# Kernel tuning notes

Measured on AMD Instinct MI355X. Metric: run time of the kernel, lower is better.

Reference implementation:

```python
import jax, jax.numpy as jnp
import numpy as np

WINDOW = 8            # window_size
P = WINDOW * WINDOW   # tokens per window = 64
DIM = 256             # feature_dim (per-token channels)
HEADS = 8
HEAD_DIM = DIM // HEADS
EPS = 1e-5


def _relative_position_index():
    # Swin-style relative position index for a WINDOW x WINDOW window.
    coords = np.stack(np.meshgrid(np.arange(WINDOW), np.arange(WINDOW), indexing='ij'))  # 2,w,w
    coords = coords.reshape(2, -1)                        # 2, P
    rel = coords[:, :, None] - coords[:, None, :]          # 2, P, P
    rel = rel.transpose(1, 2, 0)                           # P, P, 2
    rel = rel + (WINDOW - 1)
    idx = rel[:, :, 0] * (2 * WINDOW - 1) + rel[:, :, 1]   # P, P
    return idx.astype(np.int32)


def setup_inputs() -> dict:
    key = jax.random.key(0)
    ks = jax.random.split(key, 8)
    B, N, D = 8, 256, P * DIM
    x = jax.random.normal(ks[0], (B, N, D), dtype=jnp.float32)
    global_noise_info = jax.random.uniform(ks[1], (B, 1, D), dtype=jnp.float32)
    norm_gamma = jnp.ones((DIM,), jnp.float32)
    norm_beta = jnp.zeros((DIM,), jnp.float32)
    s = 1.0 / np.sqrt(DIM)
    qkv_w = jax.random.normal(ks[2], (3 * DIM, DIM), dtype=jnp.float32) * s
    proj_w = jax.random.normal(ks[3], (DIM, DIM), dtype=jnp.float32) * s
    proj_b = jnp.zeros((DIM,), jnp.float32)
    n_rel = (2 * WINDOW - 1) ** 2
    rel_bias_table = jax.random.normal(ks[4], (n_rel, HEADS), dtype=jnp.float32) * 0.02
    rel_index = jnp.asarray(_relative_position_index())  # (P, P) int32
    return {
        'x': x, 'global_noise_info': global_noise_info,
        'norm_gamma': norm_gamma, 'norm_beta': norm_beta,
        'qkv_w': qkv_w, 'proj_w': proj_w, 'proj_b': proj_b,
        'rel_bias_table': rel_bias_table, 'rel_index': rel_index,
    }


def reference(x, global_noise_info, norm_gamma, norm_beta, qkv_w, proj_w, proj_b,
              rel_bias_table, rel_index):
    B, N, D = x.shape
    d = D // P
    # elementwise noise scale + window reshape: (B, N, P*d) -> (B*N, P, d)
    xw = (x * global_noise_info).reshape(B * N, P, d)
    # LayerNorm over channel dim
    mu = jnp.mean(xw, axis=-1, keepdims=True)
    var = jnp.var(xw, axis=-1, keepdims=True)
    xn = (xw - mu) * jax.lax.rsqrt(var + EPS) * norm_gamma + norm_beta
    # qkv projection (no bias)
    qkv = jnp.einsum('wpd,ed->wpe', xn, qkv_w)                    # (BN, P, 3D)
    qkv = qkv.reshape(B * N, P, 3, HEADS, HEAD_DIM)
    q, k, v = qkv[:, :, 0], qkv[:, :, 1], qkv[:, :, 2]            # (BN, P, H, hd)
    scale = HEAD_DIM ** -0.5
    scores = jnp.einsum('wphc,wqhc->whpq', q * scale, k)          # (BN, H, P, P)
    bias = rel_bias_table[rel_index]                               # (P, P, H)
    scores = scores + jnp.transpose(bias, (2, 0, 1))[None]
    attn = jax.nn.softmax(scores, axis=-1)
    out = jnp.einsum('whpq,wqhc->wphc', attn, v).reshape(B * N, P, d)
    out = jnp.einsum('wpd,ed->wpe', out, proj_w) + proj_b
    return out.reshape(B, N, D)
```

## Files before the change

### kernel.cpp

```cpp
#include <hip/hip_runtime.h>
#include <hip/hip_fp16.h>

typedef _Float16 f16;
typedef __attribute__((ext_vector_type(8)))  f16   f16x8;
typedef __attribute__((ext_vector_type(16))) float f32x16;
typedef __attribute__((ext_vector_type(4)))  float f32x4;
typedef __attribute__((ext_vector_type(2)))  unsigned int u32x2;
typedef unsigned int uint;
typedef unsigned short ushort;

#define MFMA16 __builtin_amdgcn_mfma_f32_32x32x16_f16

#define SCALE_Q 0.17677669529663687f

#define XN_ROW   264
#define XN_BYTES (64 * XN_ROW * 2)
#define Q_OFF    XN_BYTES
#define QK_ROW   40
#define QK_HEAD  (64 * QK_ROW * 2)
#define Q_BYTES  (8 * QK_HEAD)
#define K_OFF    (Q_OFF + Q_BYTES)
#define K_BYTES  Q_BYTES
#define VT_OFF   (K_OFF + K_BYTES)
#define VT_ROW   72
#define VT_HEAD  (32 * VT_ROW * 2)
#define VT_BYTES (8 * VT_HEAD)
#define LDS_TOTAL (VT_OFF + VT_BYTES)

#define Z16 {0.f,0.f,0.f,0.f,0.f,0.f,0.f,0.f,0.f,0.f,0.f,0.f,0.f,0.f,0.f,0.f}

__device__ __forceinline__ ushort f2h_bits(float f) {
    return __builtin_bit_cast(ushort, (f16)f);
}
__device__ __forceinline__ uint pk2(float a, float b) {
    return (uint)f2h_bits(a) | ((uint)f2h_bits(b) << 16);
}

__global__ void lwa_prep(const float* __restrict__ qkvw, const float* __restrict__ projw,
                         const float* __restrict__ table, const int* __restrict__ ridx,
                         ushort* __restrict__ wq, ushort* __restrict__ wp, float* __restrict__ biasr)
{
    int i = blockIdx.x * 256 + threadIdx.x;
    if (i < 196608) {
        float v = qkvw[i];
        if (i < 65536) v *= SCALE_Q;
        wq[i] = f2h_bits(v);
    } else if (i < 262144) {
        int j = i - 196608;
        wp[j] = f2h_bits(projw[j]);
    } else {
        int j = i - 262144;
        int reg  = j & 15;
        int lane = (j >> 4) & 63;
        int nt   = (j >> 10) & 1;
        int mt   = (j >> 11) & 1;
        int h    = j >> 12;
        int qrow = nt * 32 + (lane & 31);
        int kv   = mt * 32 + (reg & 3) + 8 * (reg >> 2) + 4 * (lane >> 5);
        biasr[j] = table[ridx[qrow * 64 + kv] * 8 + h];
    }
}

__global__ __launch_bounds__(512, 2) void lwa_main(
    const float* __restrict__ x, const float* __restrict__ nz,
    const float* __restrict__ gamma, const float* __restrict__ beta,
    const ushort* __restrict__ wq, const ushort* __restrict__ wp,
    const float* __restrict__ biasr, const float* __restrict__ projb,
    float* __restrict__ out)
{
    extern __shared__ char smem[];
    const int tid  = threadIdx.x;
    const int wid  = tid >> 6;
    const int lane = tid & 63;
    const int l31  = lane & 31;
    const int h5   = lane >> 5;
    const int w    = blockIdx.x;
    const int bidx = w >> 8;
    const int kb   = h5 * 8;

    {
        const int p   = tid >> 3;
        const int sub = tid & 7;
        const float* xrow = x  + (size_t)w * 16384 + p * 256;
        const float* nrow = nz + (size_t)bidx * 16384 + p * 256;
        f32x4 v[8];
        float s = 0.f, ss = 0.f;
#pragma unroll
        for (int i = 0; i < 8; ++i) {
            const int c4 = sub + 8 * i;
            f32x4 xv = *(const f32x4*)(xrow + 4 * c4);
            f32x4 nv = *(const f32x4*)(nrow + 4 * c4);
            f32x4 t = xv * nv;
            v[i] = t;
            s  += t[0] + t[1] + t[2] + t[3];
            ss += t[0]*t[0] + t[1]*t[1] + t[2]*t[2] + t[3]*t[3];
        }
#pragma unroll
        for (int m = 1; m < 8; m <<= 1) { s += __shfl_xor(s, m, 64); ss += __shfl_xor(ss, m, 64); }
        const float mu = s * (1.f / 256.f);
        const float rs = rsqrtf(fmaxf(ss * (1.f / 256.f) - mu * mu, 0.f) + 1e-5f);
        char* xnrow = smem + (size_t)p * (XN_ROW * 2);
#pragma unroll
        for (int i = 0; i < 8; ++i) {
            const int c4 = sub + 8 * i;
            f32x4 g  = *(const f32x4*)(gamma + 4 * c4);
            f32x4 bb = *(const f32x4*)(beta  + 4 * c4);
            f32x4 t  = v[i];
            u32x2 pkv;
            pkv[0] = pk2((t[0]-mu)*rs*g[0] + bb[0], (t[1]-mu)*rs*g[1] + bb[1]);
            pkv[1] = pk2((t[2]-mu)*rs*g[2] + bb[2], (t[3]-mu)*rs*g[3] + bb[3]);
            *(u32x2*)(xnrow + c4 * 8) = pkv;
        }
    }
    __syncthreads();

    {
        f32x16 aq[2] = {Z16, Z16}, ak[2] = {Z16, Z16}, av[2] = {Z16, Z16};
        const char* xb = smem;
        const ushort* wrq = wq + (size_t)(      32 * wid + l31) * 256;
        const ushort* wrk = wq + (size_t)(256 + 32 * wid + l31) * 256;
        const ushort* wrv = wq + (size_t)(512 + 32 * wid + l31) * 256;
#pragma unroll 4
        for (int ks = 0; ks < 16; ++ks) {
            const int kk = ks * 16 + kb;
            f16x8 a0 = *(const f16x8*)(xb + ( l31       * XN_ROW + kk) * 2);
            f16x8 a1 = *(const f16x8*)(xb + ((32 + l31) * XN_ROW + kk) * 2);
            f16x8 bq = *(const f16x8*)(wrq + kk);
            f16x8 bk = *(const f16x8*)(wrk + kk);
            f16x8 bv = *(const f16x8*)(wrv + kk);
            aq[0] = MFMA16(a0, bq, aq[0], 0, 0, 0);
            aq[1] = MFMA16(a1, bq, aq[1], 0, 0, 0);
            ak[0] = MFMA16(a0, bk, ak[0], 0, 0, 0);
            ak[1] = MFMA16(a1, bk, ak[1], 0, 0, 0);
            av[0] = MFMA16(a0, bv, av[0], 0, 0, 0);
            av[1] = MFMA16(a1, bv, av[1], 0, 0, 0);
        }
        char* qh = smem + Q_OFF  + wid * QK_HEAD;
        char* kh = smem + K_OFF  + wid * QK_HEAD;
        char* vh = smem + VT_OFF + wid * VT_HEAD;
#pragma unroll
        for (int mt = 0; mt < 2; ++mt) {
#pragma unroll
            for (int r = 0; r < 16; ++r) {
                const int prow = 32 * mt + (r & 3) + 8 * (r >> 2) + 4 * h5;
                *(ushort*)(qh + (prow * QK_ROW + l31) * 2) = f2h_bits(aq[mt][r]);
                *(ushort*)(kh + (prow * QK_ROW + l31) * 2) = f2h_bits(ak[mt][r]);
            }
#pragma unroll
            for (int sg = 0; sg < 4; ++sg) {
                const int kvr = 32 * mt + 8 * sg + 4 * h5;
                u32x2 pv2;
                pv2[0] = pk2(av[mt][4*sg+0], av[mt][4*sg+1]);
                pv2[1] = pk2(av[mt][4*sg+2], av[mt][4*sg+3]);
                *(u32x2*)(vh + (l31 * VT_ROW + kvr) * 2) = pv2;
            }
        }
    }
    __syncthreads();

    {
        const int h = wid;
        const char* qh = smem + Q_OFF  + h * QK_HEAD;
        const char* kh = smem + K_OFF  + h * QK_HEAD;
        const char* vh = smem + VT_OFF + h * VT_HEAD;

        f32x16 st[2][2] = {{Z16, Z16}, {Z16, Z16}};
#pragma unroll
        for (int ks = 0; ks < 2; ++ks) {
            const int cc = ks * 16 + kb;
            f16x8 ka0 = *(const f16x8*)(kh + ( l31       * QK_ROW + cc) * 2);
            f16x8 ka1 = *(const f16x8*)(kh + ((32 + l31) * QK_ROW + cc) * 2);
            f16x8 qb0 = *(const f16x8*)(qh + ( l31       * QK_ROW + cc) * 2);
            f16x8 qb1 = *(const f16x8*)(qh + ((32 + l31) * QK_ROW + cc) * 2);
            st[0][0] = MFMA16(ka0, qb0, st[0][0], 0, 0, 0);
            st[0][1] = MFMA16(ka0, qb1, st[0][1], 0, 0, 0);
            st[1][0] = MFMA16(ka1, qb0, st[1][0], 0, 0, 0);
            st[1][1] = MFMA16(ka1, qb1, st[1][1], 0, 0, 0);
        }
#pragma unroll
        for (int mt = 0; mt < 2; ++mt)
#pragma unroll
        for (int nt = 0; nt < 2; ++nt) {
            const float* bp = biasr + ((((h * 2 + mt) * 2 + nt) * 64) + lane) * 16;
#pragma unroll
            for (int q4 = 0; q4 < 4; ++q4) {
                f32x4 bv = *(const f32x4*)(bp + 4 * q4);
                st[mt][nt][4*q4+0] += bv[0];
                st[mt][nt][4*q4+1] += bv[1];
                st[mt][nt][4*q4+2] += bv[2];
                st[mt][nt][4*q4+3] += bv[3];
            }
        }
#pragma unroll
        for (int nt = 0; nt < 2; ++nt) {
            float mx = st[0][nt][0];
#pragma unroll
            for (int mt = 0; mt < 2; ++mt)
#pragma unroll
            for (int r = 0; r < 16; ++r) mx = fmaxf(mx, st[mt][nt][r]);
            mx = fmaxf(mx, __shfl_xor(mx, 32, 64));
            float sum = 0.f;
#pragma unroll
            for (int mt = 0; mt < 2; ++mt)
#pragma unroll
            for (int r = 0; r < 16; ++r) {
                float e = __expf(st[mt][nt][r] - mx);
                st[mt][nt][r] = e;
                sum += e;
            }
            sum += __shfl_xor(sum, 32, 64);
            const float rd = __builtin_amdgcn_rcpf(sum);
#pragma unroll
            for (int mt = 0; mt < 2; ++mt)
#pragma unroll
            for (int r = 0; r < 16; ++r) st[mt][nt][r] *= rd;
        }
        uint Wd[2][2][4][2];
#pragma unroll
        for (int nt = 0; nt < 2; ++nt)
#pragma unroll
        for (int mt = 0; mt < 2; ++mt)
#pragma unroll
        for (int sg = 0; sg < 4; ++sg) {
            Wd[nt][mt][sg][0] = pk2(st[mt][nt][4*sg+0], st[mt][nt][4*sg+1]);
            Wd[nt][mt][sg][1] = pk2(st[mt][nt][4*sg+2], st[mt][nt][4*sg+3]);
        }
        f32x16 o[2] = {Z16, Z16};
#pragma unroll
        for (int ks = 0; ks < 4; ++ks) {
            f16x8 bV = *(const f16x8*)(vh + (l31 * VT_ROW + ks * 16 + kb) * 2);
            const int mt = ks >> 1;
            const int sk = 2 * (ks & 1);
#pragma unroll
            for (int nt = 0; nt < 2; ++nt) {
                const uint lo0 = Wd[nt][mt][sk + 0][0], lo1 = Wd[nt][mt][sk + 0][1];
                const uint hi0 = Wd[nt][mt][sk + 1][0], hi1 = Wd[nt][mt][sk + 1][1];
                const uint s0 = h5 ? lo0 : hi0;
                const uint s1 = h5 ? lo1 : hi1;
                const uint r0 = (uint)__shfl_xor((int)s0, 32, 64);
                const uint r1 = (uint)__shfl_xor((int)s1, 32, 64);
                union { uint u[4]; f16x8 v; } A;
                A.u[0] = h5 ? r0 : lo0;
                A.u[1] = h5 ? r1 : lo1;
                A.u[2] = h5 ? hi0 : r0;
                A.u[3] = h5 ? hi1 : r1;
                o[nt] = MFMA16(A.v, bV, o[nt], 0, 0, 0);
            }
        }
        char* ao = smem;
#pragma unroll
        for (int nt = 0; nt < 2; ++nt)
#pragma unroll
        for (int r = 0; r < 16; ++r) {
            const int row = 32 * nt + (r & 3) + 8 * (r >> 2) + 4 * h5;
            *(ushort*)(ao + (row * XN_ROW + h * 32 + l31) * 2) = f2h_bits(o[nt][r]);
        }
    }
    __syncthreads();

    {
        const ushort* wr = wp + (size_t)(32 * wid + l31) * 256;
        const char* ao = smem;
        f32x16 pa[2] = {Z16, Z16};
#pragma unroll 4
        for (int ks = 0; ks < 16; ++ks) {
            const int kk = ks * 16 + kb;
            f16x8 a0 = *(const f16x8*)(ao + ( l31       * XN_ROW + kk) * 2);
            f16x8 a1 = *(const f16x8*)(ao + ((32 + l31) * XN_ROW + kk) * 2);
            f16x8 bw = *(const f16x8*)(wr + kk);
            pa[0] = MFMA16(a0, bw, pa[0], 0, 0, 0);
            pa[1] = MFMA16(a1, bw, pa[1], 0, 0, 0);
        }
        const float pb = projb[32 * wid + l31];
        float* orow = out + (size_t)w * 16384;
#pragma unroll
        for (int mt = 0; mt < 2; ++mt)
#pragma unroll
        for (int r = 0; r < 16; ++r) {
            const int prow = 32 * mt + (r & 3) + 8 * (r >> 2) + 4 * h5;
            orow[(size_t)prow * 256 + 32 * wid + l31] = pa[mt][r] + pb;
        }
    }
}

extern "C" void kernel_launch(void* const* d_in, const int* in_sizes, int n_in,
                              void* d_out, int out_size, void* d_ws, size_t ws_size,
                              hipStream_t stream)
{
    const float* x     = (const float*)d_in[0];
    const float* nz    = (const float*)d_in[1];
    const float* gamma = (const float*)d_in[2];
    const float* beta  = (const float*)d_in[3];
    const float* qkvw  = (const float*)d_in[4];
    const float* projw = (const float*)d_in[5];
    const float* projb = (const float*)d_in[6];
    const float* table = (const float*)d_in[7];
    const int*   ridx  = (const int*)d_in[8];

    ushort* wqb   = (ushort*)d_ws;
    ushort* wpb   = wqb + 196608;
    float*  biasr = (float*)(wpb + 65536);

    (void)hipFuncSetAttribute((const void*)lwa_main,
                              hipFuncAttributeMaxDynamicSharedMemorySize, LDS_TOTAL);

    lwa_prep<<<1152, 256, 0, stream>>>(qkvw, projw, table, ridx, wqb, wpb, biasr);
    lwa_main<<<2048, 512, LDS_TOTAL, stream>>>(x, nz, gamma, beta, wqb, wpb, biasr, projb,
                                               (float*)d_out);
}
```

Measured before the change: 218.3 us.

## Keep Q/K/V attention fragments in registers and shrink LDS to raise occupancy

Q, K and V no longer pass through shared memory. The QKV projection computes Q and K transposed (weights as the A operand) and then turns the accumulators straight into MFMA input fragments using a cross-half lane shuffle. V is computed after the softmax, and its accumulator is reshuffled the same way for the PV product. Shared memory shrinks to the normalized-input buffer alone, and launch bounds rise to 4 blocks per CU to cut LDS traffic and a barrier while raising occupancy. The cost is higher register pressure under the tighter launch bound, which could cause spills, plus round-toward-zero fp16 conversions that slightly change rounding.

```diff
diff --git a/kernel.cpp b/kernel.cpp
--- a/kernel.cpp
+++ b/kernel.cpp
@@ -2,6 +2,7 @@
 #include <hip/hip_fp16.h>
 
 typedef _Float16 f16;
+typedef __attribute__((ext_vector_type(2)))  __fp16 fp16x2;
 typedef __attribute__((ext_vector_type(8)))  f16   f16x8;
 typedef __attribute__((ext_vector_type(16))) float f32x16;
 typedef __attribute__((ext_vector_type(4)))  float f32x4;
@@ -10,22 +11,10 @@
 typedef unsigned short ushort;
 
 #define MFMA16 __builtin_amdgcn_mfma_f32_32x32x16_f16
-
 #define SCALE_Q 0.17677669529663687f
 
 #define XN_ROW   264
 #define XN_BYTES (64 * XN_ROW * 2)
-#define Q_OFF    XN_BYTES
-#define QK_ROW   40
-#define QK_HEAD  (64 * QK_ROW * 2)
-#define Q_BYTES  (8 * QK_HEAD)
-#define K_OFF    (Q_OFF + Q_BYTES)
-#define K_BYTES  Q_BYTES
-#define VT_OFF   (K_OFF + K_BYTES)
-#define VT_ROW   72
-#define VT_HEAD  (32 * VT_ROW * 2)
-#define VT_BYTES (8 * VT_HEAD)
-#define LDS_TOTAL (VT_OFF + VT_BYTES)
 
 #define Z16 {0.f,0.f,0.f,0.f,0.f,0.f,0.f,0.f,0.f,0.f,0.f,0.f,0.f,0.f,0.f,0.f}
 
@@ -34,6 +23,27 @@
 }
 __device__ __forceinline__ uint pk2(float a, float b) {
     return (uint)f2h_bits(a) | ((uint)f2h_bits(b) << 16);
+}
+__device__ __forceinline__ uint pkrtz(float a, float b) {
+    fp16x2 h = __builtin_amdgcn_cvt_pkrtz(a, b);
+    return __builtin_bit_cast(uint, h);
+}
+
+__device__ __forceinline__ f16x8 build_frag(const f32x16 c, const int kss, const int h5) {
+    const int kb8 = 8 * kss;
+    const uint keep0 = pkrtz(c[kb8 + 4*h5 + 0], c[kb8 + 4*h5 + 1]);
+    const uint keep1 = pkrtz(c[kb8 + 4*h5 + 2], c[kb8 + 4*h5 + 3]);
+    const int  o     = kb8 + 4*(1 - h5);
+    const uint send0 = pkrtz(c[o + 0], c[o + 1]);
+    const uint send1 = pkrtz(c[o + 2], c[o + 3]);
+    const uint recv0 = (uint)__shfl_xor((int)send0, 32, 64);
+    const uint recv1 = (uint)__shfl_xor((int)send1, 32, 64);
+    union { uint u[4]; f16x8 v; } A;
+    A.u[0] = h5 ? recv0 : keep0;
+    A.u[1] = h5 ? recv1 : keep1;
+    A.u[2] = h5 ? keep0 : recv0;
+    A.u[3] = h5 ? keep1 : recv1;
+    return A.v;
 }
 
 __global__ void lwa_prep(const float* __restrict__ qkvw, const float* __restrict__ projw,
@@ -61,14 +71,14 @@
     }
 }
 
-__global__ __launch_bounds__(512, 2) void lwa_main(
+__global__ __launch_bounds__(512, 4) void lwa_main(
     const float* __restrict__ x, const float* __restrict__ nz,
     const float* __restrict__ gamma, const float* __restrict__ beta,
     const ushort* __restrict__ wq, const ushort* __restrict__ wp,
     const float* __restrict__ biasr, const float* __restrict__ projb,
     float* __restrict__ out)
 {
-    extern __shared__ char smem[];
+    __shared__ char smem[XN_BYTES];
     const int tid  = threadIdx.x;
     const int wid  = tid >> 6;
     const int lane = tid & 63;
@@ -114,12 +124,13 @@
     }
     __syncthreads();
 
-    {
-        f32x16 aq[2] = {Z16, Z16}, ak[2] = {Z16, Z16}, av[2] = {Z16, Z16};
-        const char* xb = smem;
+    const char* xb = smem;
+
+    f16x8 qf[2][2], kf[2][2];
+    {
+        f32x16 cq[2] = {Z16, Z16}, ck[2] = {Z16, Z16};
         const ushort* wrq = wq + (size_t)(      32 * wid + l31) * 256;
         const ushort* wrk = wq + (size_t)(256 + 32 * wid + l31) * 256;
-        const ushort* wrv = wq + (size_t)(512 + 32 * wid + l31) * 256;
 #pragma unroll 4
         for (int ks = 0; ks < 16; ++ks) {
             const int kk = ks * 16 + kb;
@@ -127,61 +138,36 @@
             f16x8 a1 = *(const f16x8*)(xb + ((32 + l31) * XN_ROW + kk) * 2);
             f16x8 bq = *(const f16x8*)(wrq + kk);
             f16x8 bk = *(const f16x8*)(wrk + kk);
-            f16x8 bv = *(const f16x8*)(wrv + kk);
-            aq[0] = MFMA16(a0, bq, aq[0], 0, 0, 0);
-            aq[1] = MFMA16(a1, bq, aq[1], 0, 0, 0);
-            ak[0] = MFMA16(a0, bk, ak[0], 0, 0, 0);
-            ak[1] = MFMA16(a1, bk, ak[1], 0, 0, 0);
-            av[0] = MFMA16(a0, bv, av[0], 0, 0, 0);
-            av[1] = MFMA16(a1, bv, av[1], 0, 0, 0);
-        }
-        char* qh = smem + Q_OFF  + wid * QK_HEAD;
-        char* kh = smem + K_OFF  + wid * QK_HEAD;
-        char* vh = smem + VT_OFF + wid * VT_HEAD;
-#pragma unroll
-        for (int mt = 0; mt < 2; ++mt) {
-#pragma unroll
-            for (int r = 0; r < 16; ++r) {
-                const int prow = 32 * mt + (r & 3) + 8 * (r >> 2) + 4 * h5;
-                *(ushort*)(qh + (prow * QK_ROW + l31) * 2) = f2h_bits(aq[mt][r]);
-                *(ushort*)(kh + (prow * QK_ROW + l31) * 2) = f2h_bits(ak[mt][r]);
-            }
-#pragma unroll
-            for (int sg = 0; sg < 4; ++sg) {
-                const int kvr = 32 * mt + 8 * sg + 4 * h5;
-                u32x2 pv2;
-                pv2[0] = pk2(av[mt][4*sg+0], av[mt][4*sg+1]);
-                pv2[1] = pk2(av[mt][4*sg+2], av[mt][4*sg+3]);
-                *(u32x2*)(vh + (l31 * VT_ROW + kvr) * 2) = pv2;
-            }
-        }
-    }
-    __syncthreads();
-
-    {
-        const int h = wid;
-        const char* qh = smem + Q_OFF  + h * QK_HEAD;
-        const char* kh = smem + K_OFF  + h * QK_HEAD;
-        const char* vh = smem + VT_OFF + h * VT_HEAD;
-
+            cq[0] = MFMA16(bq, a0, cq[0], 0, 0, 0);
+            cq[1] = MFMA16(bq, a1, cq[1], 0, 0, 0);
+            ck[0] = MFMA16(bk, a0, ck[0], 0, 0, 0);
+            ck[1] = MFMA16(bk, a1, ck[1], 0, 0, 0);
+        }
+#pragma unroll
+        for (int t = 0; t < 2; ++t)
+#pragma unroll
+        for (int ks = 0; ks < 2; ++ks) {
+            qf[t][ks] = build_frag(cq[t], ks, h5);
+            kf[t][ks] = build_frag(ck[t], ks, h5);
+        }
+    }
+
+    f16x8 pf[4][2];
+    {
         f32x16 st[2][2] = {{Z16, Z16}, {Z16, Z16}};
 #pragma unroll
-        for (int ks = 0; ks < 2; ++ks) {
-            const int cc = ks * 16 + kb;
-            f16x8 ka0 = *(const f16x8*)(kh + ( l31       * QK_ROW + cc) * 2);
-            f16x8 ka1 = *(const f16x8*)(kh + ((32 + l31) * QK_ROW + cc) * 2);
-            f16x8 qb0 = *(const f16x8*)(qh + ( l31       * QK_ROW + cc) * 2);
-            f16x8 qb1 = *(const f16x8*)(qh + ((32 + l31) * QK_ROW + cc) * 2);
-            st[0][0] = MFMA16(ka0, qb0, st[0][0], 0, 0, 0);
-            st[0][1] = MFMA16(ka0, qb1, st[0][1], 0, 0, 0);
-            st[1][0] = MFMA16(ka1, qb0, st[1][0], 0, 0, 0);
-            st[1][1] = MFMA16(ka1, qb1, st[1][1], 0, 0, 0);
-        }
-#pragma unroll
         for (int mt = 0; mt < 2; ++mt)
 #pragma unroll
+        for (int nt = 0; nt < 2; ++nt)
+#pragma unroll
+        for (int ks = 0; ks < 2; ++ks)
+            st[mt][nt] = MFMA16(kf[mt][ks], qf[nt][ks], st[mt][nt], 0, 0, 0);
+
+#pragma unroll
+        for (int mt = 0; mt < 2; ++mt)
+#pragma unroll
         for (int nt = 0; nt < 2; ++nt) {
-            const float* bp = biasr + ((((h * 2 + mt) * 2 + nt) * 64) + lane) * 16;
+            const float* bp = biasr + ((((wid * 2 + mt) * 2 + nt) * 64) + lane) * 16;
 #pragma unroll
             for (int q4 = 0; q4 < 4; ++q4) {
                 f32x4 bv = *(const f32x4*)(bp + 4 * q4);
@@ -215,45 +201,45 @@
 #pragma unroll
             for (int r = 0; r < 16; ++r) st[mt][nt][r] *= rd;
         }
-        uint Wd[2][2][4][2];
-#pragma unroll
-        for (int nt = 0; nt < 2; ++nt)
-#pragma unroll
-        for (int mt = 0; mt < 2; ++mt)
-#pragma unroll
-        for (int sg = 0; sg < 4; ++sg) {
-            Wd[nt][mt][sg][0] = pk2(st[mt][nt][4*sg+0], st[mt][nt][4*sg+1]);
-            Wd[nt][mt][sg][1] = pk2(st[mt][nt][4*sg+2], st[mt][nt][4*sg+3]);
-        }
-        f32x16 o[2] = {Z16, Z16};
-#pragma unroll
-        for (int ks = 0; ks < 4; ++ks) {
-            f16x8 bV = *(const f16x8*)(vh + (l31 * VT_ROW + ks * 16 + kb) * 2);
-            const int mt = ks >> 1;
-            const int sk = 2 * (ks & 1);
-#pragma unroll
-            for (int nt = 0; nt < 2; ++nt) {
-                const uint lo0 = Wd[nt][mt][sk + 0][0], lo1 = Wd[nt][mt][sk + 0][1];
-                const uint hi0 = Wd[nt][mt][sk + 1][0], hi1 = Wd[nt][mt][sk + 1][1];
-                const uint s0 = h5 ? lo0 : hi0;
-                const uint s1 = h5 ? lo1 : hi1;
-                const uint r0 = (uint)__shfl_xor((int)s0, 32, 64);
-                const uint r1 = (uint)__shfl_xor((int)s1, 32, 64);
-                union { uint u[4]; f16x8 v; } A;
-                A.u[0] = h5 ? r0 : lo0;
-                A.u[1] = h5 ? r1 : lo1;
-                A.u[2] = h5 ? hi0 : r0;
-                A.u[3] = h5 ? hi1 : r1;
-                o[nt] = MFMA16(A.v, bV, o[nt], 0, 0, 0);
-            }
-        }
+#pragma unroll
+        for (int ks = 0; ks < 4; ++ks)
+#pragma unroll
+        for (int nt = 0; nt < 2; ++nt)
+            pf[ks][nt] = build_frag(st[ks >> 1][nt], ks & 1, h5);
+    }
+
+    f32x16 av[2] = {Z16, Z16};
+    {
+        const ushort* wrv = wq + (size_t)(512 + 32 * wid + l31) * 256;
+#pragma unroll 4
+        for (int ks = 0; ks < 16; ++ks) {
+            const int kk = ks * 16 + kb;
+            f16x8 a0 = *(const f16x8*)(xb + ( l31       * XN_ROW + kk) * 2);
+            f16x8 a1 = *(const f16x8*)(xb + ((32 + l31) * XN_ROW + kk) * 2);
+            f16x8 bv = *(const f16x8*)(wrv + kk);
+            av[0] = MFMA16(a0, bv, av[0], 0, 0, 0);
+            av[1] = MFMA16(a1, bv, av[1], 0, 0, 0);
+        }
+    }
+
+    f32x16 o[2] = {Z16, Z16};
+#pragma unroll
+    for (int ks = 0; ks < 4; ++ks) {
+        f16x8 vf = build_frag(av[ks >> 1], ks & 1, h5);
+#pragma unroll
+        for (int nt = 0; nt < 2; ++nt)
+            o[nt] = MFMA16(pf[ks][nt], vf, o[nt], 0, 0, 0);
+    }
+
+    __syncthreads();
+    {
         char* ao = smem;
 #pragma unroll
         for (int nt = 0; nt < 2; ++nt)
 #pragma unroll
         for (int r = 0; r < 16; ++r) {
             const int row = 32 * nt + (r & 3) + 8 * (r >> 2) + 4 * h5;
-            *(ushort*)(ao + (row * XN_ROW + h * 32 + l31) * 2) = f2h_bits(o[nt][r]);
+            *(ushort*)(ao + (row * XN_ROW + wid * 32 + l31) * 2) = f2h_bits(o[nt][r]);
         }
     }
     __syncthreads();
@@ -301,10 +287,7 @@
     ushort* wpb   = wqb + 196608;
     float*  biasr = (float*)(wpb + 65536);
 
-    (void)hipFuncSetAttribute((const void*)lwa_main,
-                              hipFuncAttributeMaxDynamicSharedMemorySize, LDS_TOTAL);
-
     lwa_prep<<<1152, 256, 0, stream>>>(qkvw, projw, table, ridx, wqb, wpb, biasr);
-    lwa_main<<<2048, 512, LDS_TOTAL, stream>>>(x, nz, gamma, beta, wqb, wpb, biasr, projb,
-                                               (float*)d_out);
-}
+    lwa_main<<<2048, 512, 0, stream>>>(x, nz, gamma, beta, wqb, wpb, biasr, projb,
+                                       (float*)d_out);
+}
```

After: 275.8 us. 26.4% more time.
